# Optimization experiments

Hardware: AMD Instinct MI355X
Metric: run time of the kernel (lower is better)

Reference implementation:

```python
import jax, jax.numpy as jnp
import numpy as np
from jax import lax

B_, L_, C_IN = 32, 1024, 3
D_MODEL, D_STATE, D_CONV, EXPAND = 256, 16, 4, 2
D_INNER = EXPAND * D_MODEL           # 512
DT_RANK = D_MODEL // 16              # 16
N_HEADS, N_CLASS = 8, 10
LN_EPS = 1e-5


def _pos_emb(L, d):
    pos = np.arange(L, dtype=np.float32)[:, None]
    div = np.exp(np.arange(0, d, 2, dtype=np.float32) * (-np.log(10000.0) / d))
    pe = np.zeros((L, d), np.float32)
    pe[:, 0::2] = np.sin(pos * div)
    pe[:, 1::2] = np.cos(pos * div)
    return jnp.asarray(pe)


def setup_inputs() -> dict:
    key = jax.random.key(0)
    ks = jax.random.split(key, 12)
    f = lambda k, shp, s: jax.random.normal(k, shp, jnp.float32) * s
    return {
        'x_enc': f(ks[0], (B_, L_, C_IN), 1.0),
        'x_mark_enc': jnp.ones((B_, L_), jnp.float32),
        'conv_emb_w': f(ks[1], (D_MODEL, C_IN, 3), (2.0 / (C_IN * 3)) ** 0.5),
        'in_proj_w': f(ks[2], (2 * D_INNER, D_MODEL), D_MODEL ** -0.5),
        'conv1d_w': f(ks[3], (D_INNER, 1, D_CONV), D_CONV ** -0.5),
        'conv1d_b': f(ks[4], (D_INNER,), 0.02),
        'x_proj_w': f(ks[5], (DT_RANK + 2 * D_STATE, D_INNER), D_INNER ** -0.5),
        'dt_proj_w': f(ks[6], (D_INNER, DT_RANK), DT_RANK ** -0.5),
        'dt_proj_b': f(ks[7], (D_INNER,), 0.1) - 2.0,
        'A_log': jnp.log(jnp.tile(jnp.arange(1, D_STATE + 1, dtype=jnp.float32), (D_INNER, 1))),
        'D': jnp.ones((D_INNER,), jnp.float32),
        'out_proj_w': f(ks[8], (D_MODEL, D_INNER), D_INNER ** -0.5),
        'ln_g': jnp.ones((D_MODEL,), jnp.float32),
        'ln_b': jnp.zeros((D_MODEL,), jnp.float32),
        'out_w': f(ks[9], (N_CLASS, D_MODEL), D_MODEL ** -0.5),
        'attn_w': f(ks[10], (N_HEADS, D_MODEL), 0.02),
        'attn_b': jnp.ones((N_HEADS,), jnp.float32),
    }


def _forward(x_enc, x_mark_enc, conv_emb_w, in_proj_w, conv1d_w, conv1d_b,
             x_proj_w, dt_proj_w, dt_proj_b, A_log, D, out_proj_w,
             ln_g, ln_b, out_w, attn_w, attn_b):
    silu = jax.nn.silu
    # --- embedding: Conv1d 'same' with replicate padding + sinusoidal PE ---
    xp = jnp.pad(x_enc, ((0, 0), (1, 1), (0, 0)), mode='edge')      # k=3 -> pad (1,1)
    x = lax.conv_general_dilated(xp.transpose(0, 2, 1), conv_emb_w, (1,), 'VALID',
                                 dimension_numbers=('NCH', 'OIH', 'NCH')).transpose(0, 2, 1)
    x = x + _pos_emb(L_, D_MODEL)[None]                              # (B,L,D)

    # --- Mamba_TimeVariant (standard Mamba selective scan) ---
    xz = jnp.einsum('bld,ed->ble', x, in_proj_w)                     # (B,L,2*Din)
    xin, z = xz[..., :D_INNER], xz[..., D_INNER:]
    # depthwise causal conv, kernel D_CONV
    xc = jnp.pad(xin.transpose(0, 2, 1), ((0, 0), (0, 0), (D_CONV - 1, 0)))
    xc = lax.conv_general_dilated(xc, conv1d_w, (1,), 'VALID',
                                  feature_group_count=D_INNER,
                                  dimension_numbers=('NCH', 'OIH', 'NCH'))
    xc = silu(xc.transpose(0, 2, 1) + conv1d_b)                      # (B,L,Din)

    dbl = jnp.einsum('bld,ed->ble', xc, x_proj_w)                    # (B,L,dt_rank+2*N)
    dtr = dbl[..., :DT_RANK]
    Bm = dbl[..., DT_RANK:DT_RANK + D_STATE]                         # (B,L,N)
    Cm = dbl[..., DT_RANK + D_STATE:]                                # (B,L,N)
    dt = jax.nn.softplus(jnp.einsum('blr,dr->bld', dtr, dt_proj_w) + dt_proj_b)
    A = -jnp.exp(A_log)                                              # (Din,N)

    def step(h, inp):
        dt_t, B_t, C_t, x_t = inp                                    # (B,Din),(B,N),(B,N),(B,Din)
        dA = jnp.exp(dt_t[..., None] * A)                            # (B,Din,N)
        h = dA * h + dt_t[..., None] * B_t[:, None, :] * x_t[..., None]
        y = jnp.einsum('bdn,bn->bd', h, C_t)
        return h, y

    h0 = jnp.zeros((B_, D_INNER, D_STATE), xc.dtype)
    inputs = (dt.transpose(1, 0, 2), Bm.transpose(1, 0, 2),
              Cm.transpose(1, 0, 2), xc.transpose(1, 0, 2))
    _, ys = lax.scan(step, h0, inputs)                               # (L,B,Din)
    y = ys.transpose(1, 0, 2) + xc * D                               # skip via D
    y = y * silu(z)
    m = jnp.einsum('bld,ed->ble', y, out_proj_w)                     # (B,L,Dmodel)

    # LayerNorm + SiLU
    mu = m.mean(-1, keepdims=True)
    var = ((m - mu) ** 2).mean(-1, keepdims=True)
    m = (m - mu) * lax.rsqrt(var + LN_EPS) * ln_g + ln_b
    m = silu(m)

    # classification head
    logit = jnp.einsum('bld,cd->blc', m, out_w) * x_mark_enc[..., None]
    s = jnp.einsum('bld,hd->blh', m, attn_w) + attn_b                # (B,L,H)
    w = jax.nn.softmax(jnp.max(s, axis=2, keepdims=True), axis=1)    # (B,L,1)
    return (logit * w).sum(1)                                        # (B,num_class)


def reference(x_enc, x_mark_enc, conv_emb_w, in_proj_w, conv1d_w, conv1d_b,
              x_proj_w, dt_proj_w, dt_proj_b, A_log, D, out_proj_w,
              ln_g, ln_b, out_w, attn_w, attn_b):
    return _forward(x_enc, x_mark_enc, conv_emb_w, in_proj_w, conv1d_w, conv1d_b,
                    x_proj_w, dt_proj_w, dt_proj_b, A_log, D, out_proj_w,
                    ln_g, ln_b, out_w, attn_w, attn_b)
```

## Files before the change

kernel.cpp:

```cpp
#include <hip/hip_runtime.h>
#include <hip/hip_bf16.h>
#include <math.h>

#define B_  32
#define L_  1024
#define CIN 3
#define DM  256
#define DI  512
#define NST 16
#define NH  8
#define NC  10
#define M_TOT (B_*L_)

typedef unsigned short u16;
typedef __attribute__((ext_vector_type(8))) short bf16x8;
typedef __attribute__((ext_vector_type(4))) float f32x4;

static __device__ __forceinline__ float sigmoidf_(float x) {
    return 1.0f / (1.0f + __expf(-x));
}
static __device__ __forceinline__ u16 f2bf(float f) {
    unsigned int u = __float_as_uint(f);
    return (u16)((u + 0x7FFF + ((u >> 16) & 1)) >> 16);
}
static __device__ __forceinline__ float bf2f(u16 u) {
    return __uint_as_float(((unsigned int)u) << 16);
}
static __device__ __forceinline__ float2 bf2x2(unsigned int u) {
    return make_float2(bf2f((u16)(u & 0xffff)), bf2f((u16)(u >> 16)));
}

static __device__ __forceinline__ void reduce8_pair(float& a, float& b) {
    asm volatile(
        "s_nop 1\n\t"
        "v_add_f32 %0, %0, %0 quad_perm:[1,0,3,2] row_mask:0xf bank_mask:0xf\n\t"
        "v_add_f32 %1, %1, %1 quad_perm:[1,0,3,2] row_mask:0xf bank_mask:0xf\n\t"
        "s_nop 1\n\t"
        "v_add_f32 %0, %0, %0 quad_perm:[2,3,0,1] row_mask:0xf bank_mask:0xf\n\t"
        "v_add_f32 %1, %1, %1 quad_perm:[2,3,0,1] row_mask:0xf bank_mask:0xf\n\t"
        "s_nop 1\n\t"
        "v_add_f32 %0, %0, %0 row_half_mirror row_mask:0xf bank_mask:0xf\n\t"
        "v_add_f32 %1, %1, %1 row_half_mirror row_mask:0xf bank_mask:0xf\n\t"
        "s_nop 1\n\t"
        : "+v"(a), "+v"(b));
}

__global__ __launch_bounds__(256) void k_cvt(const float* __restrict__ in,
        u16* __restrict__ out) {
    int i = (blockIdx.x * 256 + threadIdx.x) * 4;
    float4 v = *(const float4*)(in + i);
    ushort4 o;
    o.x = f2bf(v.x); o.y = f2bf(v.y); o.z = f2bf(v.z); o.w = f2bf(v.w);
    *(ushort4*)(out + i) = o;
}

__global__ __launch_bounds__(256) void k_embed(const float* __restrict__ xe,
        const float* __restrict__ w, u16* __restrict__ x) {
    int bl = blockIdx.x;
    int l = bl & (L_-1);
    int b = bl >> 10;
    int d = threadIdx.x;
    const float* xb = xe + (size_t)b * L_ * CIN;
    int t0 = l > 0 ? l-1 : 0;
    int t2 = l < L_-1 ? l+1 : L_-1;
    const float* w3 = w + d*9;
    float acc = 0.f;
    #pragma unroll
    for (int i = 0; i < 3; ++i) {
        acc += xb[t0*3+i] * w3[i*3+0];
        acc += xb[l *3+i] * w3[i*3+1];
        acc += xb[t2*3+i] * w3[i*3+2];
    }
    int j = d >> 1;
    float div = expf((float)(2*j) * (-logf(10000.0f)/(float)DM));
    float ang = (float)l * div;
    acc += (d & 1) ? cosf(ang) : sinf(ang);
    x[(size_t)bl*DM + d] = f2bf(acc);
}

#define GST 40
__global__ __launch_bounds__(256) void k_gemm_mfma(
        const u16* __restrict__ A, const u16* __restrict__ W,
        float* __restrict__ O1f, u16* __restrict__ O1b,
        u16* __restrict__ O2b, int M, int N, int K, int S) {
    __shared__ u16 As[128*GST];
    __shared__ u16 Bs[128*GST];
    int tid = threadIdx.x;
    int row0 = blockIdx.y * 128, col0 = blockIdx.x * 128;
    int wave = tid >> 6, lane = tid & 63;
    int wr = (wave >> 1) * 64, wc = (wave & 1) * 64;
    int l16 = lane & 15, kl = lane >> 4;
    int srow = tid >> 1, skh = (tid & 1) * 16;
    const u16* Ag = A + (size_t)(row0 + srow) * K + skh;
    const u16* Wg = W + (size_t)(col0 + srow) * K + skh;

    f32x4 acc[4][4];
    #pragma unroll
    for (int m = 0; m < 4; ++m)
        #pragma unroll
        for (int n = 0; n < 4; ++n)
            acc[m][n] = (f32x4){0.f, 0.f, 0.f, 0.f};

    for (int k0 = 0; k0 < K; k0 += 32) {
        uint4 a0 = *(const uint4*)(Ag + k0);
        uint4 a1 = *(const uint4*)(Ag + k0 + 8);
        uint4 b0 = *(const uint4*)(Wg + k0);
        uint4 b1 = *(const uint4*)(Wg + k0 + 8);
        __syncthreads();
        *(uint4*)&As[srow*GST + skh]     = a0;
        *(uint4*)&As[srow*GST + skh + 8] = a1;
        *(uint4*)&Bs[srow*GST + skh]     = b0;
        *(uint4*)&Bs[srow*GST + skh + 8] = b1;
        __syncthreads();
        bf16x8 af[4], bf[4];
        #pragma unroll
        for (int m = 0; m < 4; ++m)
            af[m] = *(const bf16x8*)&As[(wr + m*16 + l16)*GST + kl*8];
        #pragma unroll
        for (int n = 0; n < 4; ++n)
            bf[n] = *(const bf16x8*)&Bs[(wc + n*16 + l16)*GST + kl*8];
        #pragma unroll
        for (int m = 0; m < 4; ++m)
            #pragma unroll
            for (int n = 0; n < 4; ++n)
                acc[m][n] = __builtin_amdgcn_mfma_f32_16x16x32_bf16(
                                af[m], bf[n], acc[m][n], 0, 0, 0);
    }

    #pragma unroll
    for (int m = 0; m < 4; ++m) {
        int rbase = row0 + wr + m*16 + kl*4;
        #pragma unroll
        for (int n = 0; n < 4; ++n) {
            int col = col0 + wc + n*16 + l16;
            #pragma unroll
            for (int r = 0; r < 4; ++r) {
                float v = acc[m][n][r];
                if (col < S) {
                    if (O1b) O1b[(size_t)(rbase + r)*S + col] = f2bf(v);
                    else     O1f[(size_t)(rbase + r)*S + col] = v;
                } else {
                    O2b[(size_t)(rbase + r)*(N - S) + (col - S)] = f2bf(v);
                }
            }
        }
    }
}

__global__ __launch_bounds__(256) void k_conv(const u16* __restrict__ xin,
        const float* __restrict__ w, const float* __restrict__ bias,
        u16* __restrict__ xc) {
    size_t i4 = (size_t)blockIdx.x * 256 + threadIdx.x;
    int d4 = (int)(i4 & (DI/4 - 1)) * 4;
    size_t m = i4 >> 7;
    int l = (int)(m & (L_-1));
    float4 wv0 = *(const float4*)(w + (size_t)(d4+0)*4);
    float4 wv1 = *(const float4*)(w + (size_t)(d4+1)*4);
    float4 wv2 = *(const float4*)(w + (size_t)(d4+2)*4);
    float4 wv3 = *(const float4*)(w + (size_t)(d4+3)*4);
    float W[4][4] = {{wv0.x,wv0.y,wv0.z,wv0.w},{wv1.x,wv1.y,wv1.z,wv1.w},
                     {wv2.x,wv2.y,wv2.z,wv2.w},{wv3.x,wv3.y,wv3.z,wv3.w}};
    float4 acc = *(const float4*)(bias + d4);
    #pragma unroll
    for (int k = 0; k < 4; ++k) {
        int t = l + k - 3;
        if (t >= 0) {
            ushort4 xv = *(const ushort4*)(xin + (m + k - 3)*DI + d4);
            acc.x = fmaf(bf2f(xv.x), W[0][k], acc.x);
            acc.y = fmaf(bf2f(xv.y), W[1][k], acc.y);
            acc.z = fmaf(bf2f(xv.z), W[2][k], acc.z);
            acc.w = fmaf(bf2f(xv.w), W[3][k], acc.w);
        }
    }
    ushort4 r;
    r.x = f2bf(acc.x * sigmoidf_(acc.x));
    r.y = f2bf(acc.y * sigmoidf_(acc.y));
    r.z = f2bf(acc.z * sigmoidf_(acc.z));
    r.w = f2bf(acc.w * sigmoidf_(acc.w));
    *(ushort4*)(xc + m*DI + d4) = r;
}

#define XBM 128
#define XBK 16
__global__ __launch_bounds__(256) void k_xproj(const u16* __restrict__ xc,
        const float* __restrict__ wp, float* __restrict__ dbl) {
    __shared__ float As[XBK][XBM];
    __shared__ float Ws[XBK][48];
    int tid = threadIdx.x;
    int row0 = blockIdx.x * XBM;
    int lr = tid >> 1;
    int lk = (tid & 1) * 8;
    int we = tid >> 2;
    int wk = (tid & 3) * 4;
    int tx = tid & 15;
    int ty = tid >> 4;
    float acc[8][3];
    #pragma unroll
    for (int i = 0; i < 8; ++i)
        #pragma unroll
        for (int j = 0; j < 3; ++j) acc[i][j] = 0.f;

    for (int k0 = 0; k0 < DI; k0 += XBK) {
        ushort4 ab0 = *(const ushort4*)(xc + (size_t)(row0+lr)*DI + k0 + lk);
        ushort4 ab1 = *(const ushort4*)(xc + (size_t)(row0+lr)*DI + k0 + lk + 4);
        float4 w0 = make_float4(0.f,0.f,0.f,0.f);
        if (tid < 192) w0 = *(const float4*)(wp + (size_t)we*DI + k0 + wk);
        __syncthreads();
        As[lk+0][lr]=bf2f(ab0.x); As[lk+1][lr]=bf2f(ab0.y);
        As[lk+2][lr]=bf2f(ab0.z); As[lk+3][lr]=bf2f(ab0.w);
        As[lk+4][lr]=bf2f(ab1.x); As[lk+5][lr]=bf2f(ab1.y);
        As[lk+6][lr]=bf2f(ab1.z); As[lk+7][lr]=bf2f(ab1.w);
        if (tid < 192) {
            Ws[wk+0][we]=w0.x; Ws[wk+1][we]=w0.y; Ws[wk+2][we]=w0.z; Ws[wk+3][we]=w0.w;
        }
        __syncthreads();
        #pragma unroll
        for (int k = 0; k < XBK; ++k) {
            float4 av0 = *(const float4*)&As[k][ty*8];
            float4 av1 = *(const float4*)&As[k][ty*8+4];
            float w0_ = Ws[k][tx*3+0];
            float w1_ = Ws[k][tx*3+1];
            float w2_ = Ws[k][tx*3+2];
            float ar[8] = {av0.x,av0.y,av0.z,av0.w,av1.x,av1.y,av1.z,av1.w};
            #pragma unroll
            for (int i = 0; i < 8; ++i) {
                acc[i][0] = fmaf(ar[i], w0_, acc[i][0]);
                acc[i][1] = fmaf(ar[i], w1_, acc[i][1]);
                acc[i][2] = fmaf(ar[i], w2_, acc[i][2]);
            }
        }
    }
    #pragma unroll
    for (int i = 0; i < 8; ++i) {
        size_t r = row0 + ty*8 + i;
        #pragma unroll
        for (int j = 0; j < 3; ++j)
            dbl[r*48 + tx*3 + j] = acc[i][j];
    }
}

__global__ __launch_bounds__(256) void k_dtproj(const float* __restrict__ dbl,
        const float* __restrict__ dtw, const float* __restrict__ dtb,
        u16* __restrict__ dt) {
    __shared__ float wl[DI][17];
    __shared__ float rl[32][16];
    size_t m0 = (size_t)blockIdx.x * 32;
    for (int i = threadIdx.x; i < DI*16; i += 256)
        wl[i >> 4][i & 15] = dtw[i];
    for (int i = threadIdx.x; i < 32*16; i += 256)
        rl[i >> 4][i & 15] = dbl[(m0 + (i>>4))*48 + (i & 15)];
    __syncthreads();
    float b0 = dtb[threadIdx.x];
    float b1 = dtb[256 + threadIdx.x];
    for (int mm = 0; mm < 32; ++mm) {
        #pragma unroll
        for (int half = 0; half < 2; ++half) {
            int d = half*256 + threadIdx.x;
            float acc = half ? b1 : b0;
            #pragma unroll
            for (int r = 0; r < 16; ++r)
                acc = fmaf(rl[mm][r], wl[d][r], acc);
            float sp = fmaxf(acc, 0.f) + log1pf(__expf(-fabsf(acc)));
            dt[(m0+mm)*DI + d] = f2bf(sp);
        }
    }
}

#define SCAN_T 64
__global__ __launch_bounds__(256) void k_scan(const u16* __restrict__ dt,
        const u16* __restrict__ xcb, const float* __restrict__ dbl,
        const float* __restrict__ A_log, const float* __restrict__ Dp,
        const u16* __restrict__ zbf, u16* __restrict__ ybf) {
    __shared__ float4 sq4[SCAN_T*33];
    __shared__ float2 sBC2[SCAN_T*18];

    int tid = threadIdx.x;
    int wave = tid >> 6, lane = tid & 63;
    int chw = lane >> 3;
    int j   = lane & 7;
    int ch  = wave*8 + chw;
    int d0 = blockIdx.x * 32;
    int b  = blockIdx.y;
    int d  = d0 + ch;
    float Aa = -expf(A_log[(size_t)d*NST + 2*j])     * 1.44269504f;
    float Ab = -expf(A_log[(size_t)d*NST + 2*j + 1]) * 1.44269504f;
    float h0 = 0.f, h1 = 0.f;
    size_t base = (size_t)b * L_;

    int st = tid >> 2;
    int sc = (tid & 3) * 8;
    int ns = (tid & 3) * 4;
    float4 Dva = *(const float4*)(Dp + d0 + sc);
    float4 Dvb = *(const float4*)(Dp + d0 + sc + 4);

    for (int t0 = 0; t0 < L_; t0 += SCAN_T) {
        __syncthreads();
        {
            size_t row = base + t0 + st;
            uint4 dv = *(const uint4*)(dt  + row*DI + d0 + sc);
            uint4 xv = *(const uint4*)(xcb + row*DI + d0 + sc);
            uint4 zv = *(const uint4*)(zbf + row*DI + d0 + sc);
            float4 Bv = *(const float4*)(dbl + row*48 + 16 + ns);
            float4 Cv = *(const float4*)(dbl + row*48 + 32 + ns);
            float2 dt01 = bf2x2(dv.x), dt23 = bf2x2(dv.y);
            float2 dt45 = bf2x2(dv.z), dt67 = bf2x2(dv.w);
            float2 x01 = bf2x2(xv.x), x23 = bf2x2(xv.y);
            float2 x45 = bf2x2(xv.z), x67 = bf2x2(xv.w);
            float2 z01 = bf2x2(zv.x), z23 = bf2x2(zv.y);
            float2 z45 = bf2x2(zv.z), z67 = bf2x2(zv.w);
            float dtr[8] = { dt01.x, dt01.y, dt23.x, dt23.y,
                             dt45.x, dt45.y, dt67.x, dt67.y };
            float xr[8]  = { x01.x, x01.y, x23.x, x23.y,
                             x45.x, x45.y, x67.x, x67.y };
            float zr[8]  = { z01.x, z01.y, z23.x, z23.y,
                             z45.x, z45.y, z67.x, z67.y };
            float Dr[8] = { Dva.x, Dva.y, Dva.z, Dva.w,
                            Dvb.x, Dvb.y, Dvb.z, Dvb.w };
            #pragma unroll
            for (int k = 0; k < 8; ++k) {
                float g = zr[k] * sigmoidf_(zr[k]);
                sq4[st*33 + sc + k] = make_float4(dtr[k], dtr[k]*xr[k],
                                                  xr[k]*Dr[k]*g, g);
            }
            *(float4*)&sBC2[st*18 + ns]     = make_float4(Bv.x, Cv.x, Bv.y, Cv.y);
            *(float4*)&sBC2[st*18 + ns + 2] = make_float4(Bv.z, Cv.z, Bv.w, Cv.w);
        }
        __syncthreads();

        #pragma unroll 2
        for (int t2 = 0; t2 < SCAN_T/2; ++t2) {
            float4 bc0 = *(const float4*)&sBC2[(2*t2)*18 + 2*j];
            float4 bc1 = *(const float4*)&sBC2[(2*t2+1)*18 + 2*j];
            float4 q0 = sq4[(2*t2)*33 + ch];
            float4 q1 = sq4[(2*t2+1)*33 + ch];
            float dA0 = exp2f(q0.x * Aa);
            float dA1 = exp2f(q0.x * Ab);
            h0 = fmaf(dA0, h0, q0.y * bc0.x);
            h1 = fmaf(dA1, h1, q0.y * bc0.z);
            float p0 = fmaf(h1, bc0.w, h0 * bc0.y);
            dA0 = exp2f(q1.x * Aa);
            dA1 = exp2f(q1.x * Ab);
            h0 = fmaf(dA0, h0, q1.y * bc1.x);
            h1 = fmaf(dA1, h1, q1.y * bc1.z);
            float p1 = fmaf(h1, bc1.w, h0 * bc1.y);
            reduce8_pair(p0, p1);
            if (j == 0) {
                size_t row = base + t0 + 2*t2;
                ybf[row*DI + d]     = f2bf(fmaf(p0, q0.w, q0.z));
                ybf[(row+1)*DI + d] = f2bf(fmaf(p1, q1.w, q1.z));
            }
        }
    }
}

#define HBK 32
__global__ __launch_bounds__(256) void k_lnheads18(const u16* __restrict__ mb,
        const float* __restrict__ g, const float* __restrict__ bta,
        const float* __restrict__ aw, const float* __restrict__ ow,
        float* __restrict__ r18) {
    __shared__ float As[128][36];
    __shared__ float Ws[18][36];
    __shared__ float gb[DM], bb[DM];
    int tid = threadIdx.x;
    int row0 = blockIdx.x * 128;
    int sr = tid >> 1, sk = (tid & 1) * 16;
    gb[tid] = g[tid];
    bb[tid] = bta[tid];
    const u16* mrow = mb + (size_t)(row0 + sr)*DM;

    float s1 = 0.f, s2 = 0.f;
    for (int k0 = 0; k0 < DM; k0 += HBK) {
        uint4 va = *(const uint4*)(mrow + k0 + sk);
        uint4 vb = *(const uint4*)(mrow + k0 + sk + 8);
        unsigned int ua[8] = {va.x, va.y, va.z, va.w, vb.x, vb.y, vb.z, vb.w};
        #pragma unroll
        for (int q = 0; q < 8; ++q) {
            float2 p = bf2x2(ua[q]);
            s1 += p.x + p.y;
            s2 += p.x*p.x + p.y*p.y;
        }
    }
    s1 += __shfl_xor(s1, 1);
    s2 += __shfl_xor(s2, 1);
    float mu = s1 * (1.0f/DM);
    float var = fmaxf(s2 * (1.0f/DM) - mu*mu, 0.f);
    float rstd = 1.0f / sqrtf(var + 1e-5f);

    int r = tid >> 1, cb = (tid & 1) * 9;
    float acc[9];
    #pragma unroll
    for (int c = 0; c < 9; ++c) acc[c] = 0.f;

    for (int k0 = 0; k0 < DM; k0 += HBK) {
        uint4 va = *(const uint4*)(mrow + k0 + sk);
        uint4 vb = *(const uint4*)(mrow + k0 + sk + 8);
        float4 wv = make_float4(0.f,0.f,0.f,0.f);
        int wc = tid >> 3, wk = (tid & 7) * 4;
        if (tid < 144) {
            const float* wsrc = (wc < NH) ? (aw + wc*DM) : (ow + (wc-NH)*DM);
            wv = *(const float4*)(wsrc + k0 + wk);
        }
        __syncthreads();
        {
            unsigned int ua[8] = {va.x, va.y, va.z, va.w, vb.x, vb.y, vb.z, vb.w};
            #pragma unroll
            for (int q = 0; q < 8; ++q) {
                float2 p = bf2x2(ua[q]);
                int c0 = k0 + sk + 2*q;
                float o0 = (p.x - mu)*rstd*gb[c0]   + bb[c0];
                float o1 = (p.y - mu)*rstd*gb[c0+1] + bb[c0+1];
                As[sr][sk + 2*q]     = o0 * sigmoidf_(o0);
                As[sr][sk + 2*q + 1] = o1 * sigmoidf_(o1);
            }
            if (tid < 144)
                *(float4*)&Ws[wc][wk] = wv;
        }
        __syncthreads();
        #pragma unroll
        for (int k4 = 0; k4 < HBK/4; ++k4) {
            float4 av = *(const float4*)&As[r][k4*4];
            #pragma unroll
            for (int c = 0; c < 9; ++c) {
                float4 w4 = *(const float4*)&Ws[cb + c][k4*4];
                acc[c] += av.x*w4.x + av.y*w4.y + av.z*w4.z + av.w*w4.w;
            }
        }
    }
    #pragma unroll
    for (int c = 0; c < 9; ++c)
        r18[(size_t)(row0 + r)*18 + cb + c] = acc[c];
}

__global__ __launch_bounds__(256) void k_final(const float* __restrict__ r18,
        const float* __restrict__ ab, const float* __restrict__ xmark,
        float* __restrict__ out) {
    __shared__ float e[L_];
    __shared__ float red[256];
    int b = blockIdx.x;
    int tid = threadIdx.x;
    float abr[NH];
    #pragma unroll
    for (int j = 0; j < NH; ++j) abr[j] = ab[j];
    float mx = -1e30f;
    for (int l = tid; l < L_; l += 256) {
        const float* rr = r18 + ((size_t)b*L_ + l)*18;
        float sm = rr[0] + abr[0];
        #pragma unroll
        for (int j = 1; j < NH; ++j) sm = fmaxf(sm, rr[j] + abr[j]);
        e[l] = sm;
        mx = fmaxf(mx, sm);
    }
    #pragma unroll
    for (int o = 32; o > 0; o >>= 1) mx = fmaxf(mx, __shfl_xor(mx, o));
    red[tid] = mx;
    __syncthreads();
    mx = fmaxf(fmaxf(red[0], red[64]), fmaxf(red[128], red[192]));
    __syncthreads();
    float ssum = 0.f;
    for (int l = tid; l < L_; l += 256) {
        float ev = __expf(e[l] - mx);
        e[l] = ev;
        ssum += ev;
    }
    #pragma unroll
    for (int o = 32; o > 0; o >>= 1) ssum += __shfl_xor(ssum, o);
    if ((tid & 63) == 0) red[tid >> 6] = ssum;
    __syncthreads();
    float inv = 1.0f / (red[0]+red[1]+red[2]+red[3]);
    float acc[NC];
    #pragma unroll
    for (int c = 0; c < NC; ++c) acc[c] = 0.f;
    for (int l = tid; l < L_; l += 256) {
        float wl = e[l] * xmark[(size_t)b*L_ + l];
        const float* lg = r18 + ((size_t)b*L_ + l)*18 + NH;
        #pragma unroll
        for (int c = 0; c < NC; ++c) acc[c] = fmaf(wl, lg[c], acc[c]);
    }
    __syncthreads();
    for (int c = 0; c < NC; ++c) {
        red[tid] = acc[c];
        __syncthreads();
        if (tid < 64) {
            float s2 = red[tid]+red[tid+64]+red[tid+128]+red[tid+192];
            #pragma unroll
            for (int o = 32; o > 0; o >>= 1) s2 += __shfl_xor(s2, o);
            if (tid == 0) out[(size_t)b*NC + c] = s2 * inv;
        }
        __syncthreads();
    }
}

extern "C" void kernel_launch(void* const* d_in, const int* in_sizes, int n_in,
                              void* d_out, int out_size, void* d_ws, size_t ws_size,
                              hipStream_t stream) {
    const float* x_enc  = (const float*)d_in[0];
    const float* x_mark = (const float*)d_in[1];
    const float* cemb_w = (const float*)d_in[2];
    const float* inp_w  = (const float*)d_in[3];
    const float* c1_w   = (const float*)d_in[4];
    const float* c1_b   = (const float*)d_in[5];
    const float* xp_w   = (const float*)d_in[6];
    const float* dtp_w  = (const float*)d_in[7];
    const float* dtp_b  = (const float*)d_in[8];
    const float* A_log  = (const float*)d_in[9];
    const float* Dp     = (const float*)d_in[10];
    const float* outp_w = (const float*)d_in[11];
    const float* ln_g   = (const float*)d_in[12];
    const float* ln_b   = (const float*)d_in[13];
    const float* out_w  = (const float*)d_in[14];
    const float* attn_w = (const float*)d_in[15];
    const float* attn_b = (const float*)d_in[16];
    float* out = (float*)d_out;

    char* ws = (char*)d_ws;
    size_t o = 0;
    u16*   xbf  = (u16*)(ws + o);   o += (size_t)M_TOT*DM*2;
    u16*   xinb = (u16*)(ws + o);   o += (size_t)M_TOT*DI*2;
    u16*   zbf  = (u16*)(ws + o);   o += (size_t)M_TOT*DI*2;
    u16*   xcb  = (u16*)(ws + o);   o += (size_t)M_TOT*DI*2;
    u16*   ybf  = (u16*)(ws + o);   o += (size_t)M_TOT*DI*2;
    u16*   dt16 = (u16*)(ws + o);   o += (size_t)M_TOT*DI*2;
    u16*   mm16 = (u16*)(ws + o);   o += (size_t)M_TOT*DM*2;
    float* dbl  = (float*)(ws + o); o += (size_t)M_TOT*48*4;
    u16*   wbfi = (u16*)(ws + o);   o += (size_t)2*DI*DM*2;
    u16*   wbfo = (u16*)(ws + o);   o += (size_t)DM*DI*2;
    float* r18  = (float*)(ws + o); o += (size_t)M_TOT*18*4;

    k_cvt   <<<(2*DI*DM)/1024, 256, 0, stream>>>(inp_w, wbfi);
    k_cvt   <<<(DM*DI)/1024, 256, 0, stream>>>(outp_w, wbfo);
    k_embed <<<M_TOT, 256, 0, stream>>>(x_enc, cemb_w, xbf);
    k_gemm_mfma<<<dim3(8, M_TOT/128), 256, 0, stream>>>(xbf, wbfi,
                                nullptr, xinb, zbf, M_TOT, 2*DI, DM, DI);
    k_conv  <<<(M_TOT*DI/4)/256, 256, 0, stream>>>(xinb, c1_w, c1_b, xcb);
    k_xproj <<<M_TOT/XBM, 256, 0, stream>>>(xcb, xp_w, dbl);
    k_dtproj<<<M_TOT/32, 256, 0, stream>>>(dbl, dtp_w, dtp_b, dt16);
    k_scan  <<<dim3(DI/32, B_), 256, 0, stream>>>(dt16, xcb, dbl, A_log, Dp,
                                                  zbf, ybf);
    k_gemm_mfma<<<dim3(2, M_TOT/128), 256, 0, stream>>>(ybf, wbfo,
                                nullptr, mm16, zbf, M_TOT, DM, DI, DM);
    k_lnheads18<<<M_TOT/128, 256, 0, stream>>>(mm16, ln_g, ln_b, attn_w,
                                               out_w, r18);
    k_final <<<B_, 256, 0, stream>>>(r18, attn_b, x_mark, out);
}
```

Measured before the change: 440.7 us.

## Load GEMM tiles directly into LDS with XOR swizzle and merge weight conversions

The MFMA GEMM now stages its A and W tiles with global_load_lds, which copies straight from global memory into shared memory and skips the register round trip. The padded LDS stride is replaced by an unpadded layout with an XOR swizzle to avoid bank conflicts on the fragment reads. Separately, the two weight-conversion launches are merged into one kernel to save a launch. Loads are still not double-buffered, so the sync stalls remain, and the swizzle has to match exactly between the writes and the reads for the results to stay correct.

```diff
diff --git a/kernel.cpp b/kernel.cpp
--- a/kernel.cpp
+++ b/kernel.cpp
@@ -15,6 +15,8 @@
 typedef unsigned short u16;
 typedef __attribute__((ext_vector_type(8))) short bf16x8;
 typedef __attribute__((ext_vector_type(4))) float f32x4;
+typedef const __attribute__((address_space(1))) unsigned int* gptr_t;
+typedef __attribute__((address_space(3))) unsigned int* sptr_t;
 
 static __device__ __forceinline__ float sigmoidf_(float x) {
     return 1.0f / (1.0f + __expf(-x));
@@ -28,6 +30,11 @@
 }
 static __device__ __forceinline__ float2 bf2x2(unsigned int u) {
     return make_float2(bf2f((u16)(u & 0xffff)), bf2f((u16)(u >> 16)));
+}
+static __device__ __forceinline__ void gload_lds16(const void* g, void* s) {
+    __builtin_amdgcn_global_load_lds(
+        (gptr_t)(unsigned long long)g,
+        (sptr_t)(unsigned int)(unsigned long long)s, 16, 0, 0);
 }
 
 static __device__ __forceinline__ void reduce8_pair(float& a, float& b) {
@@ -45,13 +52,19 @@
         : "+v"(a), "+v"(b));
 }
 
-__global__ __launch_bounds__(256) void k_cvt(const float* __restrict__ in,
-        u16* __restrict__ out) {
-    int i = (blockIdx.x * 256 + threadIdx.x) * 4;
-    float4 v = *(const float4*)(in + i);
+__global__ __launch_bounds__(256) void k_cvt2(const float* __restrict__ wi,
+        const float* __restrict__ wo, u16* __restrict__ obi,
+        u16* __restrict__ obo) {
+    int idx = blockIdx.x * 256 + threadIdx.x;
+    const float* src;
+    u16* dst;
+    int i;
+    if (idx < (2*DI*DM)/4) { src = wi; dst = obi; i = idx*4; }
+    else { src = wo; dst = obo; i = (idx - (2*DI*DM)/4)*4; }
+    float4 v = *(const float4*)(src + i);
     ushort4 o;
     o.x = f2bf(v.x); o.y = f2bf(v.y); o.z = f2bf(v.z); o.w = f2bf(v.w);
-    *(ushort4*)(out + i) = o;
+    *(ushort4*)(dst + i) = o;
 }
 
 __global__ __launch_bounds__(256) void k_embed(const float* __restrict__ xe,
@@ -78,21 +91,20 @@
     x[(size_t)bl*DM + d] = f2bf(acc);
 }
 
-#define GST 40
+#define BKK 32
 __global__ __launch_bounds__(256) void k_gemm_mfma(
         const u16* __restrict__ A, const u16* __restrict__ W,
         float* __restrict__ O1f, u16* __restrict__ O1b,
         u16* __restrict__ O2b, int M, int N, int K, int S) {
-    __shared__ u16 As[128*GST];
-    __shared__ u16 Bs[128*GST];
+    __shared__ u16 As[128*BKK];
+    __shared__ u16 Bs[128*BKK];
     int tid = threadIdx.x;
     int row0 = blockIdx.y * 128, col0 = blockIdx.x * 128;
     int wave = tid >> 6, lane = tid & 63;
     int wr = (wave >> 1) * 64, wc = (wave & 1) * 64;
     int l16 = lane & 15, kl = lane >> 4;
-    int srow = tid >> 1, skh = (tid & 1) * 16;
-    const u16* Ag = A + (size_t)(row0 + srow) * K + skh;
-    const u16* Wg = W + (size_t)(col0 + srow) * K + skh;
+    int sr_ = lane >> 2;
+    int sc_ = lane & 3;
 
     f32x4 acc[4][4];
     #pragma unroll
@@ -101,24 +113,29 @@
         for (int n = 0; n < 4; ++n)
             acc[m][n] = (f32x4){0.f, 0.f, 0.f, 0.f};
 
-    for (int k0 = 0; k0 < K; k0 += 32) {
-        uint4 a0 = *(const uint4*)(Ag + k0);
-        uint4 a1 = *(const uint4*)(Ag + k0 + 8);
-        uint4 b0 = *(const uint4*)(Wg + k0);
-        uint4 b1 = *(const uint4*)(Wg + k0 + 8);
-        __syncthreads();
-        *(uint4*)&As[srow*GST + skh]     = a0;
-        *(uint4*)&As[srow*GST + skh + 8] = a1;
-        *(uint4*)&Bs[srow*GST + skh]     = b0;
-        *(uint4*)&Bs[srow*GST + skh + 8] = b1;
+    for (int k0 = 0; k0 < K; k0 += BKK) {
+        __syncthreads();
+        #pragma unroll
+        for (int t = 0; t < 2; ++t) {
+            int r = wave*32 + t*16 + sr_;
+            int csw = sc_ ^ ((r >> 2) & 3);
+            gload_lds16(A + (size_t)(row0 + r)*K + k0 + csw*8,
+                        &As[(wave*32 + t*16)*BKK]);
+            gload_lds16(W + (size_t)(col0 + r)*K + k0 + csw*8,
+                        &Bs[(wave*32 + t*16)*BKK]);
+        }
         __syncthreads();
         bf16x8 af[4], bf[4];
         #pragma unroll
-        for (int m = 0; m < 4; ++m)
-            af[m] = *(const bf16x8*)&As[(wr + m*16 + l16)*GST + kl*8];
-        #pragma unroll
-        for (int n = 0; n < 4; ++n)
-            bf[n] = *(const bf16x8*)&Bs[(wc + n*16 + l16)*GST + kl*8];
+        for (int m = 0; m < 4; ++m) {
+            int row = wr + m*16 + l16;
+            af[m] = *(const bf16x8*)&As[row*BKK + (kl ^ ((row>>2)&3))*8];
+        }
+        #pragma unroll
+        for (int n = 0; n < 4; ++n) {
+            int row = wc + n*16 + l16;
+            bf[n] = *(const bf16x8*)&Bs[row*BKK + (kl ^ ((row>>2)&3))*8];
+        }
         #pragma unroll
         for (int m = 0; m < 4; ++m)
             #pragma unroll
@@ -526,8 +543,8 @@
     u16*   wbfo = (u16*)(ws + o);   o += (size_t)DM*DI*2;
     float* r18  = (float*)(ws + o); o += (size_t)M_TOT*18*4;
 
-    k_cvt   <<<(2*DI*DM)/1024, 256, 0, stream>>>(inp_w, wbfi);
-    k_cvt   <<<(DM*DI)/1024, 256, 0, stream>>>(outp_w, wbfo);
+    k_cvt2  <<<(2*DI*DM + DM*DI)/1024, 256, 0, stream>>>(inp_w, outp_w,
+                                                         wbfi, wbfo);
     k_embed <<<M_TOT, 256, 0, stream>>>(x_enc, cemb_w, xbf);
     k_gemm_mfma<<<dim3(8, M_TOT/128), 256, 0, stream>>>(xbf, wbfi,
                                 nullptr, xinb, zbf, M_TOT, 2*DI, DM, DI);
```

Result: no change. 436.5 us (median of 2 runs) (-0.9%).
